# Kernel tuning notes

Hardware: AMD Instinct MI355X
Metric: run time of the kernel (lower is better)

## Reference

```python
import jax, jax.numpy as jnp
import numpy as np

B_SZ, C_IN, C_OUT, H, W = 16, 32, 32, 128, 128
K, CODE, PAD, FACTOR = 3, 2, 1, 1.0

def setup_inputs() -> dict:
    key = jax.random.key(0)
    ks = jax.random.split(key, 7)
    s = 0.05
    return {
        "x": jax.random.normal(ks[0], (B_SZ, C_IN, H, W), jnp.float32),
        "codes": jax.random.normal(ks[1], (B_SZ, CODE, CODE), jnp.float32),
        "weight": jax.random.normal(ks[2], (C_OUT, C_IN, K, K), jnp.float32) * s,
        "A": jax.random.normal(ks[3], (C_IN, CODE, K, K), jnp.float32) * s,
        "Bm": jax.random.normal(ks[4], (C_OUT, CODE, K, K), jnp.float32) * s,
        "bias": jax.random.normal(ks[5], (C_OUT,), jnp.float32) * s,
        "bias_context": jax.random.normal(ks[6], (CODE, C_OUT), jnp.float32) * s,
    }

def reference(x, codes, weight, A, Bm, bias, bias_context):
    # hypernetwork weight synthesis: [b, out, in, k, k]
    w_ctx = jnp.einsum('ickl,bcr->birkl', A, codes)            # [b, in, code, k, k]
    w_ctx = jnp.einsum('birkl,orkl->boikl', w_ctx, Bm)         # [b, out, in, k, k]
    combined_weight = weight[None] + FACTOR * w_ctx
    # per-sample bias from diagonal of codes
    diag = jnp.diagonal(codes, axis1=-2, axis2=-1)             # [b, code]
    combined_bias = bias[None] + FACTOR * (diag @ bias_context)  # [b, out]
    # circular padding then per-sample VALID conv (== unfold + einsum)
    xp = jnp.pad(x, ((0, 0), (0, 0), (PAD, PAD), (PAD, PAD)), mode='wrap')
    def conv_one(xi, wi):
        return jax.lax.conv_general_dilated(
            xi[None], wi, window_strides=(1, 1), padding='VALID',
            dimension_numbers=('NCHW', 'OIHW', 'NCHW'))[0]
    out = jax.vmap(conv_one)(xp, combined_weight)              # [b, out, H, W]
    return out + combined_bias[:, :, None, None]
```

## Files before the change

### kernel.cpp

```cpp
#include <hip/hip_runtime.h>

typedef short bf16x8 __attribute__((ext_vector_type(8)));
typedef float f32x4  __attribute__((ext_vector_type(4)));
typedef unsigned short u16;
typedef unsigned int   u32;

#define HH 128
#define WW 128

__device__ __forceinline__ u16 f2bf(float f) {
    union { float f; u32 i; } v; v.f = f;
    u32 x = v.i;
    x += 0x7fffu + ((x >> 16) & 1u);
    return (u16)(x >> 16);
}

__global__ __launch_bounds__(256, 2) void geps_mfma_kernel(
    const float* __restrict__ x, const float* __restrict__ codes,
    const float* __restrict__ weight, const float* __restrict__ A,
    const float* __restrict__ Bm, const float* __restrict__ bias,
    const float* __restrict__ bctx, float* __restrict__ out)
{
    __shared__ bf16x8 lds_x[3072];
    __shared__ bf16x8 lds_w[1152];
    __shared__ float  lds_ctx[576];
    __shared__ float  lds_b[32];

    const int tid = threadIdx.x;
    const int l   = tid & 63;
    const int wv  = tid >> 6;

    const int orig = blockIdx.x;
    const int vb   = (orig & 7) * 64 + (orig >> 3);
    const int rb   = vb & 31;
    const int b    = vb >> 5;
    const int h0   = rb * 4;

    const float c00 = codes[b * 4 + 0];
    const float c01 = codes[b * 4 + 1];
    const float c10 = codes[b * 4 + 2];
    const float c11 = codes[b * 4 + 3];

    for (int j = tid; j < 576; j += 256) {
        int i = j / 18, rem = j % 18, r = rem / 9, kl = rem % 9;
        float a0 = A[(i * 2 + 0) * 9 + kl];
        float a1 = A[(i * 2 + 1) * 9 + kl];
        lds_ctx[j] = (r == 0) ? (a0 * c00 + a1 * c10) : (a0 * c01 + a1 * c11);
    }
    if (tid < 32) lds_b[tid] = bias[tid] + c00 * bctx[tid] + c11 * bctx[32 + tid];
    __syncthreads();

    for (int j = tid; j < 1152; j += 256) {
        int kl = j >> 7, rem = j & 127, o = rem >> 2, kb = rem & 3;
        float m0 = Bm[(o * 2 + 0) * 9 + kl];
        float m1 = Bm[(o * 2 + 1) * 9 + kl];
        bf16x8 w8;
        #pragma unroll
        for (int jj = 0; jj < 8; ++jj) {
            int i = kb * 8 + jj;
            float wf = weight[(o * 32 + i) * 9 + kl]
                     + lds_ctx[(i * 2 + 0) * 9 + kl] * m0
                     + lds_ctx[(i * 2 + 1) * 9 + kl] * m1;
            w8[jj] = (short)f2bf(wf);
        }
        lds_w[kl * 128 + (o >> 4) * 64 + kb * 16 + (o & 15)] = w8;
    }

    for (int it = 0; it < 6; ++it) {
        int idx = it * 256 + tid;
        int cp  = idx & 63;
        int ig  = (idx >> 6) & 3;
        int row = idx >> 8;
        int c0  = cp * 2;
        int grow = (h0 - 1 + row) & 127;
        const float* src = x + ((size_t)(b * 32 + ig * 8) * HH + grow) * WW + c0;
        bf16x8 v0, v1;
        #pragma unroll
        for (int jj = 0; jj < 8; ++jj) {
            float2 f = *(const float2*)(src + (size_t)jj * HH * WW);
            v0[jj] = (short)f2bf(f.x);
            v1[jj] = (short)f2bf(f.y);
        }
        int didx = row * 512 + (c0 >> 4) * 64 + ig * 16 + (c0 & 15);
        lds_x[didx]     = v0;
        lds_x[didx + 1] = v1;
    }
    __syncthreads();

    const int awb = (l >> 4) * 16 + (l & 15);
    bf16x8 af[9][2];
    #pragma unroll
    for (int kl = 0; kl < 9; ++kl)
        #pragma unroll
        for (int oh = 0; oh < 2; ++oh)
            af[kl][oh] = lds_w[kl * 128 + oh * 64 + awb];

    const int p = l & 15, ig = l >> 4;
    int bb[3];
    #pragma unroll
    for (int dl = -1; dl <= 1; ++dl) {
        int pq = p + dl;
        bb[dl + 1] = (pq & 15) + ((pq >> 4) << 6) + ig * 16;
    }

    f32x4 acc[2][8];
    #pragma unroll
    for (int oh = 0; oh < 2; ++oh)
        #pragma unroll
        for (int nt = 0; nt < 8; ++nt)
            acc[oh][nt] = (f32x4){0.f, 0.f, 0.f, 0.f};

    #pragma unroll
    for (int nt = 0; nt < 8; ++nt) {
        #pragma unroll
        for (int lc = 0; lc < 3; ++lc) {
            int t = (bb[lc] + nt * 64) & 511;
            #pragma unroll
            for (int k = 0; k < 3; ++k) {
                bf16x8 bf = lds_x[(wv + k) * 512 + t];
                acc[0][nt] = __builtin_amdgcn_mfma_f32_16x16x32_bf16(
                    af[k * 3 + lc][0], bf, acc[0][nt], 0, 0, 0);
                acc[1][nt] = __builtin_amdgcn_mfma_f32_16x16x32_bf16(
                    af[k * 3 + lc][1], bf, acc[1][nt], 0, 0, 0);
            }
        }
    }

    float bl[2][4];
    #pragma unroll
    for (int oh = 0; oh < 2; ++oh)
        #pragma unroll
        for (int r = 0; r < 4; ++r)
            bl[oh][r] = lds_b[oh * 16 + (l >> 4) * 4 + r];

    const int h = h0 + wv;
    const size_t obase = ((size_t)(b * 32 + (l >> 4) * 4) * HH + h) * WW + p;
    #pragma unroll
    for (int oh = 0; oh < 2; ++oh)
        #pragma unroll
        for (int nt = 0; nt < 8; ++nt)
            #pragma unroll
            for (int r = 0; r < 4; ++r)
                out[obase + (size_t)(oh * 16 + r) * (HH * WW) + nt * 16] =
                    acc[oh][nt][r] + bl[oh][r];
}

extern "C" void kernel_launch(void* const* d_in, const int* in_sizes, int n_in,
                              void* d_out, int out_size, void* d_ws, size_t ws_size,
                              hipStream_t stream) {
    const float* x      = (const float*)d_in[0];
    const float* codes  = (const float*)d_in[1];
    const float* weight = (const float*)d_in[2];
    const float* A      = (const float*)d_in[3];
    const float* Bm     = (const float*)d_in[4];
    const float* bias   = (const float*)d_in[5];
    const float* bctx   = (const float*)d_in[6];
    float* out = (float*)d_out;

    hipLaunchKernelGGL(geps_mfma_kernel, dim3(512), dim3(256), 0, stream,
                       x, codes, weight, A, Bm, bias, bctx, out);
}
```

Measured before the change: 26.27 us.

## Split output-channel halves across waves and synthesize weights directly in registers

Doubles the block to 512 threads, giving each wave one output row and one 16-channel half instead of both halves. Each lane now builds its own bf16 weight fragments from global weight/Bm and the LDS context, dropping the LDS weight buffer and one staging pass. Weight synthesis sits before the barrier so it can overlap the x staging. In exchange, weight arithmetic is repeated across the 4 row-waves sharing an output half, and global weight reads are strided per lane.

```diff
diff --git a/kernel.cpp b/kernel.cpp
--- a/kernel.cpp
+++ b/kernel.cpp
@@ -15,20 +15,21 @@
     return (u16)(x >> 16);
 }
 
-__global__ __launch_bounds__(256, 2) void geps_mfma_kernel(
+__global__ __launch_bounds__(512, 4) void geps_mfma_kernel(
     const float* __restrict__ x, const float* __restrict__ codes,
     const float* __restrict__ weight, const float* __restrict__ A,
     const float* __restrict__ Bm, const float* __restrict__ bias,
     const float* __restrict__ bctx, float* __restrict__ out)
 {
     __shared__ bf16x8 lds_x[3072];
-    __shared__ bf16x8 lds_w[1152];
     __shared__ float  lds_ctx[576];
     __shared__ float  lds_b[32];
 
     const int tid = threadIdx.x;
     const int l   = tid & 63;
-    const int wv  = tid >> 6;
+    const int wvid = tid >> 6;
+    const int row = wvid >> 1;
+    const int oh  = wvid & 1;
 
     const int orig = blockIdx.x;
     const int vb   = (orig & 7) * 64 + (orig >> 3);
@@ -41,7 +42,7 @@
     const float c10 = codes[b * 4 + 2];
     const float c11 = codes[b * 4 + 3];
 
-    for (int j = tid; j < 576; j += 256) {
+    for (int j = tid; j < 576; j += 512) {
         int i = j / 18, rem = j % 18, r = rem / 9, kl = rem % 9;
         float a0 = A[(i * 2 + 0) * 9 + kl];
         float a1 = A[(i * 2 + 1) * 9 + kl];
@@ -50,29 +51,14 @@
     if (tid < 32) lds_b[tid] = bias[tid] + c00 * bctx[tid] + c11 * bctx[32 + tid];
     __syncthreads();
 
-    for (int j = tid; j < 1152; j += 256) {
-        int kl = j >> 7, rem = j & 127, o = rem >> 2, kb = rem & 3;
-        float m0 = Bm[(o * 2 + 0) * 9 + kl];
-        float m1 = Bm[(o * 2 + 1) * 9 + kl];
-        bf16x8 w8;
-        #pragma unroll
-        for (int jj = 0; jj < 8; ++jj) {
-            int i = kb * 8 + jj;
-            float wf = weight[(o * 32 + i) * 9 + kl]
-                     + lds_ctx[(i * 2 + 0) * 9 + kl] * m0
-                     + lds_ctx[(i * 2 + 1) * 9 + kl] * m1;
-            w8[jj] = (short)f2bf(wf);
-        }
-        lds_w[kl * 128 + (o >> 4) * 64 + kb * 16 + (o & 15)] = w8;
-    }
-
-    for (int it = 0; it < 6; ++it) {
-        int idx = it * 256 + tid;
+    #pragma unroll
+    for (int it = 0; it < 3; ++it) {
+        int idx = it * 512 + tid;
         int cp  = idx & 63;
         int ig  = (idx >> 6) & 3;
-        int row = idx >> 8;
+        int rr  = idx >> 8;
         int c0  = cp * 2;
-        int grow = (h0 - 1 + row) & 127;
+        int grow = (h0 - 1 + rr) & 127;
         const float* src = x + ((size_t)(b * 32 + ig * 8) * HH + grow) * WW + c0;
         bf16x8 v0, v1;
         #pragma unroll
@@ -81,34 +67,42 @@
             v0[jj] = (short)f2bf(f.x);
             v1[jj] = (short)f2bf(f.y);
         }
-        int didx = row * 512 + (c0 >> 4) * 64 + ig * 16 + (c0 & 15);
+        int didx = rr * 512 + (c0 >> 4) * 64 + ig * 16 + (c0 & 15);
         lds_x[didx]     = v0;
         lds_x[didx + 1] = v1;
     }
+
+    const int o_l = oh * 16 + (l & 15);
+    const int i0  = (l >> 4) * 8;
+    bf16x8 af[9];
+    #pragma unroll
+    for (int kl = 0; kl < 9; ++kl) {
+        float m0 = Bm[(o_l * 2 + 0) * 9 + kl];
+        float m1 = Bm[(o_l * 2 + 1) * 9 + kl];
+        bf16x8 w8;
+        #pragma unroll
+        for (int jj = 0; jj < 8; ++jj) {
+            int i = i0 + jj;
+            float wf = weight[(o_l * 32 + i) * 9 + kl]
+                     + lds_ctx[i * 18 + kl] * m0
+                     + lds_ctx[i * 18 + 9 + kl] * m1;
+            w8[jj] = (short)f2bf(wf);
+        }
+        af[kl] = w8;
+    }
     __syncthreads();
 
-    const int awb = (l >> 4) * 16 + (l & 15);
-    bf16x8 af[9][2];
-    #pragma unroll
-    for (int kl = 0; kl < 9; ++kl)
-        #pragma unroll
-        for (int oh = 0; oh < 2; ++oh)
-            af[kl][oh] = lds_w[kl * 128 + oh * 64 + awb];
-
-    const int p = l & 15, ig = l >> 4;
+    const int p = l & 15, igf = l >> 4;
     int bb[3];
     #pragma unroll
     for (int dl = -1; dl <= 1; ++dl) {
         int pq = p + dl;
-        bb[dl + 1] = (pq & 15) + ((pq >> 4) << 6) + ig * 16;
+        bb[dl + 1] = (pq & 15) + ((pq >> 4) << 6) + igf * 16;
     }
 
-    f32x4 acc[2][8];
+    f32x4 acc[8];
     #pragma unroll
-    for (int oh = 0; oh < 2; ++oh)
-        #pragma unroll
-        for (int nt = 0; nt < 8; ++nt)
-            acc[oh][nt] = (f32x4){0.f, 0.f, 0.f, 0.f};
+    for (int nt = 0; nt < 8; ++nt) acc[nt] = (f32x4){0.f, 0.f, 0.f, 0.f};
 
     #pragma unroll
     for (int nt = 0; nt < 8; ++nt) {
@@ -117,32 +111,24 @@
             int t = (bb[lc] + nt * 64) & 511;
             #pragma unroll
             for (int k = 0; k < 3; ++k) {
-                bf16x8 bf = lds_x[(wv + k) * 512 + t];
-                acc[0][nt] = __builtin_amdgcn_mfma_f32_16x16x32_bf16(
-                    af[k * 3 + lc][0], bf, acc[0][nt], 0, 0, 0);
-                acc[1][nt] = __builtin_amdgcn_mfma_f32_16x16x32_bf16(
-                    af[k * 3 + lc][1], bf, acc[1][nt], 0, 0, 0);
+                bf16x8 bfv = lds_x[(row + k) * 512 + t];
+                acc[nt] = __builtin_amdgcn_mfma_f32_16x16x32_bf16(
+                    af[k * 3 + lc], bfv, acc[nt], 0, 0, 0);
             }
         }
     }
 
-    float bl[2][4];
+    float blr[4];
     #pragma unroll
-    for (int oh = 0; oh < 2; ++oh)
+    for (int r = 0; r < 4; ++r) blr[r] = lds_b[oh * 16 + (l >> 4) * 4 + r];
+
+    const int h = h0 + row;
+    const size_t obase = ((size_t)(b * 32 + oh * 16 + (l >> 4) * 4) * HH + h) * WW + p;
+    #pragma unroll
+    for (int nt = 0; nt < 8; ++nt)
         #pragma unroll
         for (int r = 0; r < 4; ++r)
-            bl[oh][r] = lds_b[oh * 16 + (l >> 4) * 4 + r];
-
-    const int h = h0 + wv;
-    const size_t obase = ((size_t)(b * 32 + (l >> 4) * 4) * HH + h) * WW + p;
-    #pragma unroll
-    for (int oh = 0; oh < 2; ++oh)
-        #pragma unroll
-        for (int nt = 0; nt < 8; ++nt)
-            #pragma unroll
-            for (int r = 0; r < 4; ++r)
-                out[obase + (size_t)(oh * 16 + r) * (HH * WW) + nt * 16] =
-                    acc[oh][nt][r] + bl[oh][r];
+            out[obase + (size_t)r * (HH * WW) + nt * 16] = acc[nt][r] + blr[r];
 }
 
 extern "C" void kernel_launch(void* const* d_in, const int* in_sizes, int n_in,
@@ -157,6 +143,6 @@
     const float* bctx   = (const float*)d_in[6];
     float* out = (float*)d_out;
 
-    hipLaunchKernelGGL(geps_mfma_kernel, dim3(512), dim3(256), 0, stream,
+    hipLaunchKernelGGL(geps_mfma_kernel, dim3(512), dim3(512), 0, stream,
                        x, codes, weight, A, Bm, bias, bctx, out);
 }
```

Result: slower. 52.35 us (+99.3%).
